# Kernel tuning notes

Hardware: AMD Instinct MI355X
Metric: run time of the kernel (lower is better)

## Reference

```python
import jax, jax.numpy as jnp
import numpy as np

P = 128; D = 128; A = 128
NS = D * A            # sinogram nodes
NP = P * P            # pixel nodes
N = NS + NP           # total graph nodes
EPS = 1e-5
_PNAMES = ["af_w1","af_b1","af_p1","af_bn_g","af_bn_b","af_w2","af_b2","af_p2","af_w3","af_b3","af_p3","af_w4","af_b4","af_p4","af_w5","af_b5","af_p5","gcn_w","gcn_b","sr_w1","sr_b1","sr_p1","sr_w2","sr_b2","sr_p2","sr_w3","sr_b3","sr_p3"]


def _conv(x, w, b, pad):
    y = jax.lax.conv_general_dilated(x, w, (1, 1), [(pad, pad), (pad, pad)],
                                     dimension_numbers=("NCHW", "OIHW", "NCHW"))
    return y + b[None, :, None, None]


def _prelu(x, a):
    return jnp.where(x >= 0, x, a * x)


def _bn(x, g, b):
    # BatchNorm2d in training mode: biased batch stats over (N,H,W)
    m = x.mean(axis=(0, 2, 3), keepdims=True)
    v = x.var(axis=(0, 2, 3), keepdims=True)
    return (x - m) * jax.lax.rsqrt(v + EPS) * g[None, :, None, None] + b[None, :, None, None]


def _forward(sino, edge_index, edge_weight, p):
    # AndrewCNN sinogram filter: 1 -> 64 -> 64 -> 64 -> 64 -> 8, 7x7 convs
    h = _prelu(_conv(sino, p["af_w1"], p["af_b1"], 3), p["af_p1"])
    h = _bn(h, p["af_bn_g"], p["af_bn_b"])
    h = _prelu(_conv(h, p["af_w2"], p["af_b2"], 3), p["af_p2"])
    h = _prelu(_conv(h, p["af_w3"], p["af_b3"], 3), p["af_p3"])
    h = _prelu(_conv(h, p["af_w4"], p["af_b4"], 3), p["af_p4"])
    h = _prelu(_conv(h, p["af_w5"], p["af_b5"], 3), p["af_p5"])   # [B,8,D,A]
    B, F = h.shape[0], h.shape[1]
    # build_nodes_features (source_to_target): sino nodes first, zero pixel nodes
    flat_sino = h.transpose(0, 2, 3, 1).reshape(B, NS, F)
    x = jnp.concatenate([flat_sino, jnp.zeros((B, NP, F), h.dtype)], axis=1)  # [B,N,8]
    # GCNConv(8,10): lin -> gcn_norm with self loops -> scatter-add at targets -> +bias
    xl = x @ p["gcn_w"]                                            # [B,N,10]
    row, col = edge_index[0], edge_index[1]
    loop = jnp.arange(N)
    row2 = jnp.concatenate([row, loop])
    col2 = jnp.concatenate([col, loop])
    w2 = jnp.concatenate([edge_weight, jnp.ones((N,), edge_weight.dtype)])
    deg = jnp.zeros((N,), xl.dtype).at[col2].add(w2)
    dis = jnp.where(deg > 0, jax.lax.rsqrt(jnp.maximum(deg, EPS * 0 + 1e-30)), 0.0)
    norm = dis[row2] * w2 * dis[col2]                              # [E+N]
    msgs = xl[:, row2, :] * norm[None, :, None]                    # [B,E+N,10]
    agg = jnp.zeros_like(xl).at[:, col2, :].add(msgs) + p["gcn_b"]
    # keep pixel nodes, reshape to image grid
    img = agg[:, NS:, :].transpose(0, 2, 1).reshape(B, -1, P, P)   # [B,10,P,P]
    # SRNET: 10 -> 64 (9x9) -> 32 (1x1) -> 1 (5x5)
    o = _prelu(_conv(img, p["sr_w1"], p["sr_b1"], 4), p["sr_p1"])
    o = _prelu(_conv(o,   p["sr_w2"], p["sr_b2"], 0), p["sr_p2"])
    o = _prelu(_conv(o,   p["sr_w3"], p["sr_b3"], 2), p["sr_p3"])
    return o


def setup_inputs() -> dict:
    f = jnp.float32
    ks = jax.random.split(jax.random.key(0), 16)
    B, E = 4, 2097152
    def rn(k, shape, s):
        return jax.random.normal(k, shape, f) * s
    inp = {
        "sino": jax.random.normal(ks[0], (B, 1, D, A), f),
        "edge_index": jax.random.randint(ks[1], (2, E), 0, N),
        "edge_weight": jax.random.uniform(ks[2], (E,), f),
    }
    kw = jax.random.split(ks[3], 9)
    inp["af_w1"] = rn(kw[0], (64, 1, 7, 7), 0.2)
    inp["af_w2"] = rn(kw[1], (64, 64, 7, 7), 0.03)
    inp["af_w3"] = rn(kw[2], (64, 64, 7, 7), 0.03)
    inp["af_w4"] = rn(kw[3], (64, 64, 7, 7), 0.03)
    inp["af_w5"] = rn(kw[4], (8, 64, 7, 7), 0.03)
    inp["gcn_w"] = rn(kw[5], (8, 10), 0.3)
    inp["sr_w1"] = rn(kw[6], (64, 10, 9, 9), 0.05)
    inp["sr_w2"] = rn(kw[7], (32, 64, 1, 1), 0.18)
    inp["sr_w3"] = rn(kw[8], (1, 32, 5, 5), 0.05)
    for nm, c in [("af_b1", 64), ("af_b2", 64), ("af_b3", 64), ("af_b4", 64), ("af_b5", 8), ("sr_b1", 64), ("sr_b2", 32), ("sr_b3", 1)]:
        inp[nm] = jnp.zeros((c,), f)
    inp["gcn_b"] = jnp.zeros((10,), f)
    inp["af_bn_g"] = jnp.ones((64,), f)
    inp["af_bn_b"] = jnp.zeros((64,), f)
    for nm in ["af_p1", "af_p2", "af_p3", "af_p4", "af_p5", "sr_p1", "sr_p2", "sr_p3"]:
        inp[nm] = jnp.array(0.25, f)
    return inp


def reference(sino, edge_index, edge_weight, af_w1, af_b1, af_p1, af_bn_g, af_bn_b, af_w2, af_b2, af_p2, af_w3, af_b3, af_p3, af_w4, af_b4, af_p4, af_w5, af_b5, af_p5, gcn_w, gcn_b, sr_w1, sr_b1, sr_p1, sr_w2, sr_b2, sr_p2, sr_w3, sr_b3, sr_p3):
    p = dict(zip(_PNAMES, (af_w1, af_b1, af_p1, af_bn_g, af_bn_b, af_w2, af_b2, af_p2, af_w3, af_b3, af_p3, af_w4, af_b4, af_p4, af_w5, af_b5, af_p5, gcn_w, gcn_b, sr_w1, sr_b1, sr_p1, sr_w2, sr_b2, sr_p2, sr_w3, sr_b3, sr_p3)))
    return _forward(sino, edge_index, edge_weight, p)
```

## Files before the change

kernel.cpp:

```cpp
#include <hip/hip_runtime.h>

static constexpr int NS = 16384;

typedef __attribute__((ext_vector_type(8))) short bf16x8;
typedef __attribute__((ext_vector_type(4))) float f32x4;

__device__ inline unsigned short bf16_rne(float x) {
  unsigned u = __float_as_uint(x);
  unsigned r = u + 0x7FFF + ((u >> 16) & 1);
  return (unsigned short)(r >> 16);
}

__global__ void k_wtrans(const float* __restrict__ w, float* __restrict__ wT,
                         int CO, int CI_IN, int CI_OUT, int KS) {
  int i = blockIdx.x * 256 + threadIdx.x;
  int tot = KS * KS * CI_OUT * CO;
  if (i >= tot) return;
  int co = i % CO;
  int r = i / CO;
  int ci = r % CI_OUT;
  int t = r / CI_OUT;
  int ky = t / KS, kx = t % KS;
  float v = 0.f;
  if (ci < CI_IN) v = w[((co * CI_IN + ci) * KS + ky) * KS + kx];
  wT[i] = v;
}

__global__ void k_wpack(const float* __restrict__ w, unsigned short* __restrict__ wpk) {
  int i = blockIdx.x * 256 + threadIdx.x;
  if (i >= 49 * 64 * 64) return;
  int co = i & 63, r = i >> 6;
  int ci = r & 63, tap = r >> 6;
  float v = w[(co * 64 + ci) * 49 + tap];
  unsigned short hi = bf16_rne(v);
  float hif = __uint_as_float((unsigned)hi << 16);
  unsigned short lo = bf16_rne(v - hif);
  int ks = ci >> 5, k32 = ci & 31;
  int lane = ((k32 >> 3) << 4) | (co & 15);
  int j = ci & 7, nt = co >> 4;
  size_t base = ((size_t)(((tap * 2 + ks) * 4 + nt) * 2) * 64 + lane) * 8 + j;
  wpk[base] = hi;
  wpk[base + 512] = lo;
}

__global__ void k_wpacks(const float* __restrict__ sw1,
                         unsigned short* __restrict__ wpk) {
  int i = blockIdx.x * 256 + threadIdx.x;
  if (i >= 360 * 512) return;
  int j = i & 7, l = (i >> 3) & 63, f = i >> 9;
  int sp = f & 1, nt = (f >> 1) & 3;
  int r3 = f >> 3, p = r3 % 5, ky = r3 / 5;
  int co = nt * 16 + (l & 15);
  int k = ((l >> 4) << 3) + j;
  int kx = 2 * p + (k >> 4);
  int ci = k & 15;
  float v = (ci < 10 && kx < 9) ? sw1[((co * 10 + ci) * 9 + ky) * 9 + kx] : 0.f;
  unsigned short hi = bf16_rne(v);
  unsigned short outv;
  if (sp == 0) {
    outv = hi;
  } else {
    float hif = __uint_as_float((unsigned)hi << 16);
    outv = bf16_rne(v - hif);
  }
  wpk[i] = outv;
}

__global__ __launch_bounds__(128) void k_conv1(
    const float* __restrict__ sino, const float* __restrict__ wT1,
    const float* __restrict__ b1, const float* __restrict__ p1,
    float* __restrict__ out) {
  int b = blockIdx.x >> 7, y = blockIdx.x & 127, x = threadIdx.x;
  float acc[64];
#pragma unroll
  for (int i = 0; i < 64; ++i) acc[i] = 0.f;
#pragma unroll
  for (int ky = 0; ky < 7; ++ky) {
    int yy = y + ky - 3;
#pragma unroll
    for (int kx = 0; kx < 7; ++kx) {
      int xx = x + kx - 3;
      float v = (yy >= 0 && yy < 128 && xx >= 0 && xx < 128)
                    ? sino[(b * 128 + yy) * 128 + xx]
                    : 0.f;
      const float* wr = wT1 + (ky * 7 + kx) * 64;
#pragma unroll
      for (int co = 0; co < 64; ++co) acc[co] += v * wr[co];
    }
  }
  float a = p1[0];
  float* op = out + ((size_t)(b * 134 + y + 3) * 134 + x + 3) * 64;
#pragma unroll
  for (int co = 0; co < 64; ++co) {
    float v = acc[co] + b1[co];
    op[co] = v >= 0.f ? v : a * v;
  }
}

__global__ __launch_bounds__(256) void k_bnstats(const float* __restrict__ x1p,
                                                 double* __restrict__ bnsum) {
  int c = threadIdx.x & 63, sl = threadIdx.x >> 6;
  double s = 0.0, q = 0.0;
  int base = blockIdx.x * 512 + sl * 128;
  for (int i = 0; i < 128; ++i) {
    int p = base + i;
    int b = p >> 14, y = (p >> 7) & 127, x = p & 127;
    double v = (double)x1p[((size_t)(b * 134 + y + 3) * 134 + x + 3) * 64 + c];
    s += v;
    q += v * v;
  }
  __shared__ double red[2][4][64];
  red[0][sl][c] = s;
  red[1][sl][c] = q;
  __syncthreads();
  if (sl == 0) {
    s = red[0][0][c] + red[0][1][c] + red[0][2][c] + red[0][3][c];
    q = red[1][0][c] + red[1][1][c] + red[1][2][c] + red[1][3][c];
    atomicAdd(&bnsum[c], s);
    atomicAdd(&bnsum[64 + c], q);
  }
}

__global__ void k_bnfinal(const double* __restrict__ bnsum, float* __restrict__ bnsc,
                          const float* __restrict__ g, const float* __restrict__ bb) {
  int c = threadIdx.x;
  if (c >= 64) return;
  double m = bnsum[c] * (1.0 / 65536.0);
  double v = bnsum[64 + c] * (1.0 / 65536.0) - m * m;
  double sc = (double)g[c] * rsqrt(v + 1e-5);
  bnsc[c] = (float)sc;
  bnsc[64 + c] = (float)((double)bb[c] - m * sc);
}

__global__ __launch_bounds__(256) void k_bnapply(float* __restrict__ x1p,
                                                 const float* __restrict__ bnsc) {
  int i = blockIdx.x * 256 + threadIdx.x;
  if (i >= 4 * 128 * 128 * 16) return;
  int g = i & 15, p = i >> 4;
  int b = p >> 14, y = (p >> 7) & 127, x = p & 127;
  float* ptr = x1p + ((size_t)(b * 134 + y + 3) * 134 + x + 3) * 64 + g * 4;
  float4 v = *(float4*)ptr;
  int c = g * 4;
  v.x = v.x * bnsc[c + 0] + bnsc[64 + c + 0];
  v.y = v.y * bnsc[c + 1] + bnsc[64 + c + 1];
  v.z = v.z * bnsc[c + 2] + bnsc[64 + c + 2];
  v.w = v.w * bnsc[c + 3] + bnsc[64 + c + 3];
  *(float4*)ptr = v;
}

__global__ __launch_bounds__(256) void k_convm(
    const float* __restrict__ in, const unsigned short* __restrict__ wpk,
    const float* __restrict__ bias, const float* __restrict__ alpha,
    float* __restrict__ out) {
  int b = blockIdx.x >> 7, y = blockIdx.x & 127;
  int tid = threadIdx.x, l = tid & 63;
  int wv = tid >> 6;
  int wbase = wv * 32;
  int lg = l >> 4, lm = l & 15;

  __shared__ unsigned short hbuf[2][134 * 40];
  __shared__ unsigned short lbuf[2][134 * 40];

  f32x4 acc[2][4];
#pragma unroll
  for (int mt = 0; mt < 2; ++mt)
#pragma unroll
    for (int nt = 0; nt < 4; ++nt) acc[mt][nt] = (f32x4){0.f, 0.f, 0.f, 0.f};

  for (int ch = 0; ch < 64; ch += 32) {
    auto stage = [&](int ky, int s) {
      const float* gin = in + ((size_t)(b * 134 + y + ky) * 134) * 64 + ch;
      for (int i = tid; i < 134 * 8; i += 256) {
        int px = i >> 3, q = i & 7;
        float4 v = *(const float4*)(gin + px * 64 + q * 4);
        unsigned short h0 = bf16_rne(v.x), h1 = bf16_rne(v.y);
        unsigned short h2 = bf16_rne(v.z), h3 = bf16_rne(v.w);
        unsigned short l0 = bf16_rne(v.x - __uint_as_float((unsigned)h0 << 16));
        unsigned short l1 = bf16_rne(v.y - __uint_as_float((unsigned)h1 << 16));
        unsigned short l2 = bf16_rne(v.z - __uint_as_float((unsigned)h2 << 16));
        unsigned short l3 = bf16_rne(v.w - __uint_as_float((unsigned)h3 << 16));
        *(ushort4*)&hbuf[s][px * 40 + q * 4] = make_ushort4(h0, h1, h2, h3);
        *(ushort4*)&lbuf[s][px * 40 + q * 4] = make_ushort4(l0, l1, l2, l3);
      }
    };
    stage(0, 0);
    __syncthreads();
    for (int ky = 0; ky < 7; ++ky) {
      if (ky < 6) stage(ky + 1, (ky + 1) & 1);
      int s = ky & 1;
#pragma unroll
      for (int kx = 0; kx < 7; ++kx) {
        int tap = ky * 7 + kx;
        const unsigned short* wt =
            wpk + (size_t)(tap * 2 + (ch >> 5)) * 8 * 512 + (size_t)l * 8;
        bf16x8 Bh[4], Bl[4];
#pragma unroll
        for (int nt = 0; nt < 4; ++nt) {
          Bh[nt] = *(const bf16x8*)(wt + (nt * 2 + 0) * 512);
          Bl[nt] = *(const bf16x8*)(wt + (nt * 2 + 1) * 512);
        }
#pragma unroll
        for (int mt = 0; mt < 2; ++mt) {
          int px = wbase + mt * 16 + lm + kx;
          bf16x8 Ah = *(const bf16x8*)&hbuf[s][px * 40 + lg * 8];
          bf16x8 Al = *(const bf16x8*)&lbuf[s][px * 40 + lg * 8];
#pragma unroll
          for (int nt = 0; nt < 4; ++nt) {
            acc[mt][nt] =
                __builtin_amdgcn_mfma_f32_16x16x32_bf16(Ah, Bh[nt], acc[mt][nt], 0, 0, 0);
            acc[mt][nt] =
                __builtin_amdgcn_mfma_f32_16x16x32_bf16(Ah, Bl[nt], acc[mt][nt], 0, 0, 0);
            acc[mt][nt] =
                __builtin_amdgcn_mfma_f32_16x16x32_bf16(Al, Bh[nt], acc[mt][nt], 0, 0, 0);
          }
        }
      }
      __syncthreads();
    }
  }
  float a = alpha[0];
#pragma unroll
  for (int mt = 0; mt < 2; ++mt)
#pragma unroll
    for (int nt = 0; nt < 4; ++nt)
#pragma unroll
      for (int r = 0; r < 4; ++r) {
        int px = wbase + mt * 16 + lg * 4 + r;
        int co = nt * 16 + lm;
        float v = acc[mt][nt][r] + bias[co];
        out[((size_t)(b * 134 + y + 3) * 134 + px + 3) * 64 + co] =
            v >= 0.f ? v : a * v;
      }
}

__global__ __launch_bounds__(256) void k_convs(
    const float* __restrict__ imgp, const unsigned short* __restrict__ wpk,
    const float* __restrict__ bias, const float* __restrict__ alpha,
    float* __restrict__ out) {
  int b = blockIdx.x >> 7, y = blockIdx.x & 127;
  int tid = threadIdx.x, l = tid & 63;
  int wv = tid >> 6, wbase = wv * 32;
  int lg = l >> 4, lm = l & 15;

  __shared__ unsigned short hbuf[2][137 * 20];
  __shared__ unsigned short lbuf[2][137 * 20];

  f32x4 acc[2][4];
#pragma unroll
  for (int mt = 0; mt < 2; ++mt)
#pragma unroll
    for (int nt = 0; nt < 4; ++nt) acc[mt][nt] = (f32x4){0.f, 0.f, 0.f, 0.f};

  auto stage = [&](int ky, int s) {
    const float* gin = imgp + ((size_t)(b * 136 + y + ky) * 136) * 16;
    for (int i = tid; i < 137 * 4; i += 256) {
      int px = i >> 2, q = i & 3;
      float4 v = (px < 136) ? *(const float4*)(gin + px * 16 + q * 4)
                            : make_float4(0.f, 0.f, 0.f, 0.f);
      unsigned short h0 = bf16_rne(v.x), h1 = bf16_rne(v.y);
      unsigned short h2 = bf16_rne(v.z), h3 = bf16_rne(v.w);
      unsigned short l0 = bf16_rne(v.x - __uint_as_float((unsigned)h0 << 16));
      unsigned short l1 = bf16_rne(v.y - __uint_as_float((unsigned)h1 << 16));
      unsigned short l2 = bf16_rne(v.z - __uint_as_float((unsigned)h2 << 16));
      unsigned short l3 = bf16_rne(v.w - __uint_as_float((unsigned)h3 << 16));
      *(ushort4*)&hbuf[s][px * 20 + q * 4] = make_ushort4(h0, h1, h2, h3);
      *(ushort4*)&lbuf[s][px * 20 + q * 4] = make_ushort4(l0, l1, l2, l3);
    }
  };
  stage(0, 0);
  __syncthreads();
  for (int ky = 0; ky < 9; ++ky) {
    if (ky < 8) stage(ky + 1, (ky + 1) & 1);
    int s = ky & 1;
#pragma unroll
    for (int p = 0; p < 5; ++p) {
      const unsigned short* wt =
          wpk + ((size_t)(ky * 5 + p) * 8) * 512 + (size_t)l * 8;
      bf16x8 Bh[4], Bl[4];
#pragma unroll
      for (int nt = 0; nt < 4; ++nt) {
        Bh[nt] = *(const bf16x8*)(wt + (nt * 2 + 0) * 512);
        Bl[nt] = *(const bf16x8*)(wt + (nt * 2 + 1) * 512);
      }
#pragma unroll
      for (int mt = 0; mt < 2; ++mt) {
        int px = wbase + mt * 16 + lm + 2 * p + (lg >> 1);
        bf16x8 Ah = *(const bf16x8*)&hbuf[s][px * 20 + (lg & 1) * 8];
        bf16x8 Al = *(const bf16x8*)&lbuf[s][px * 20 + (lg & 1) * 8];
#pragma unroll
        for (int nt = 0; nt < 4; ++nt) {
          acc[mt][nt] =
              __builtin_amdgcn_mfma_f32_16x16x32_bf16(Ah, Bh[nt], acc[mt][nt], 0, 0, 0);
          acc[mt][nt] =
              __builtin_amdgcn_mfma_f32_16x16x32_bf16(Ah, Bl[nt], acc[mt][nt], 0, 0, 0);
          acc[mt][nt] =
              __builtin_amdgcn_mfma_f32_16x16x32_bf16(Al, Bh[nt], acc[mt][nt], 0, 0, 0);
        }
      }
    }
    __syncthreads();
  }
  float a = alpha[0];
#pragma unroll
  for (int mt = 0; mt < 2; ++mt)
#pragma unroll
    for (int nt = 0; nt < 4; ++nt)
#pragma unroll
      for (int r = 0; r < 4; ++r) {
        int px = wbase + mt * 16 + lg * 4 + r;
        int co = nt * 16 + lm;
        float v = acc[mt][nt][r] + bias[co];
        out[((size_t)(b * 128 + y) * 128 + px) * 64 + co] = v >= 0.f ? v : a * v;
      }
}

template <int CIN, int COUT, int KS, int IN_H, int IN_W, int OUT_H, int OUT_W,
          int OUT_OFF, int STR, int CH, int NSPLIT>
__global__ __launch_bounds__(64 * NSPLIT) void k_conv3(
    const float* __restrict__ in, const float* __restrict__ wT,
    const float* __restrict__ bias, const float* __restrict__ alpha,
    float* __restrict__ out) {
  constexpr int C = COUT / NSPLIT;
  int b = blockIdx.x >> 6, y0 = (blockIdx.x & 63) * 2;
  int l = threadIdx.x & 63;
  int cob = __builtin_amdgcn_readfirstlane((int)(threadIdx.x >> 6) * C);
  __shared__ float sbuf[2][IN_W * STR];
  float acc[4][C];
#pragma unroll
  for (int r = 0; r < 4; ++r)
#pragma unroll
    for (int i = 0; i < C; ++i) acc[r][i] = 0.f;

  for (int ch = 0; ch < CIN; ch += CH) {
    auto stage = [&](int k) {
      const float* gin = in + ((size_t)(b * IN_H + y0 + k) * IN_W) * CIN + ch;
      float* dst = sbuf[k & 1];
      constexpr int N4 = IN_W * CH / 4;
      for (int i = threadIdx.x; i < N4; i += 64 * NSPLIT) {
        int xx = i / (CH / 4), c4 = (i - xx * (CH / 4)) * 4;
        float4 v = *(const float4*)(gin + (size_t)xx * CIN + c4);
        *(float4*)(dst + xx * STR + c4) = v;
      }
    };
    stage(0);
    stage(1);
    __syncthreads();
    for (int ky = 0; ky < KS; ++ky) {
      const float* sA = sbuf[ky & 1];
      const float* sB = sbuf[(ky + 1) & 1];
      for (int kx = 0; kx < KS; ++kx) {
        const float* wt = wT + ((size_t)(ky * KS + kx) * CIN + ch) * COUT + cob;
        const float* a0p = sA + (l + kx) * STR;
        const float* a1p = sA + (l + 64 + kx) * STR;
        const float* b0p = sB + (l + kx) * STR;
        const float* b1p = sB + (l + 64 + kx) * STR;
#pragma unroll
        for (int ci = 0; ci < CH; ci += 4) {
          float4 a0 = *(const float4*)(a0p + ci);
          float4 a1 = *(const float4*)(a1p + ci);
          float4 b0 = *(const float4*)(b0p + ci);
          float4 b1 = *(const float4*)(b1p + ci);
#pragma unroll
          for (int c = 0; c < 4; ++c) {
            const float* wr = wt + (size_t)(ci + c) * COUT;
            float va0 = ((const float*)&a0)[c], va1 = ((const float*)&a1)[c];
            float vb0 = ((const float*)&b0)[c], vb1 = ((const float*)&b1)[c];
#pragma unroll
            for (int co = 0; co < C; ++co) {
              float w = wr[co];
              acc[0][co] += va0 * w;
              acc[1][co] += va1 * w;
              acc[2][co] += vb0 * w;
              acc[3][co] += vb1 * w;
            }
          }
        }
      }
      __syncthreads();
      if (ky < KS - 1) {
        stage(ky + 2);
        __syncthreads();
      }
    }
  }
  float a = alpha[0];
#pragma unroll
  for (int r = 0; r < 2; ++r) {
    float* rowp =
        out + (((size_t)(b * OUT_H + y0 + r + OUT_OFF)) * OUT_W + OUT_OFF) * COUT + cob;
#pragma unroll
    for (int p = 0; p < 2; ++p) {
      float* op = rowp + (size_t)(l + p * 64) * COUT;
#pragma unroll
      for (int co = 0; co < C; ++co) {
        float v = acc[r * 2 + p][co] + bias[cob + co];
        op[co] = v >= 0.f ? v : a * v;
      }
    }
  }
}

template <int CIN, int COUT, int KS, int IN_H, int IN_W, int OUT_H, int OUT_W,
          int OUT_OFF, int STR, int NSPLIT>
__global__ __launch_bounds__(64 * NSPLIT) void k_conv2(
    const float* __restrict__ in, const float* __restrict__ wT,
    const float* __restrict__ bias, const float* __restrict__ alpha,
    float* __restrict__ out) {
  constexpr int C = COUT / NSPLIT;
  int b = blockIdx.x >> 7, y = blockIdx.x & 127;
  int l = threadIdx.x & 63;
  int cob = __builtin_amdgcn_readfirstlane((int)(threadIdx.x >> 6) * C);
  __shared__ float srow[IN_W * STR];
  float acc0[C], acc1[C];
#pragma unroll
  for (int i = 0; i < C; ++i) acc0[i] = acc1[i] = 0.f;

  for (int ky = 0; ky < KS; ++ky) {
    __syncthreads();
    const float* gin = in + (size_t)(b * IN_H + y + ky) * IN_W * CIN;
    constexpr int N4 = IN_W * CIN / 4;
    for (int i = threadIdx.x; i < N4; i += 64 * NSPLIT) {
      float4 v = *(const float4*)(gin + (size_t)i * 4);
      int xx = (i * 4) / CIN, cc = (i * 4) % CIN;
      *(float4*)(srow + xx * STR + cc) = v;
    }
    __syncthreads();
    for (int kx = 0; kx < KS; ++kx) {
      const float* wt = wT + ((size_t)(ky * KS + kx) * CIN) * COUT + cob;
      const float* s0 = srow + (l + kx) * STR;
      const float* s1 = srow + (l + 64 + kx) * STR;
      for (int ci = 0; ci < CIN; ci += 4) {
        float4 a0 = *(const float4*)(s0 + ci);
        float4 a1 = *(const float4*)(s1 + ci);
#pragma unroll
        for (int c = 0; c < 4; ++c) {
          float v0 = ((const float*)&a0)[c];
          float v1 = ((const float*)&a1)[c];
          const float* wr = wt + (size_t)(ci + c) * COUT;
#pragma unroll
          for (int co = 0; co < C; ++co) {
            float w = wr[co];
            acc0[co] += v0 * w;
            acc1[co] += v1 * w;
          }
        }
      }
    }
  }
  float a = alpha[0];
  float* rowp = out + ((size_t)(b * OUT_H + y + OUT_OFF) * OUT_W + OUT_OFF) * COUT + cob;
  float* op0 = rowp + (size_t)l * COUT;
  float* op1 = rowp + (size_t)(l + 64) * COUT;
#pragma unroll
  for (int co = 0; co < C; ++co) {
    float bi = bias[cob + co];
    float v0 = acc0[co] + bi;
    float v1 = acc1[co] + bi;
    op0[co] = v0 >= 0.f ? v0 : a * v0;
    op1[co] = v1 >= 0.f ? v1 : a * v1;
  }
}

__global__ __launch_bounds__(512, 4) void k_conv5gcn(
    const float* __restrict__ in, const float* __restrict__ wT5,
    const float* __restrict__ b5, const float* __restrict__ p5,
    const float* __restrict__ gw, float* __restrict__ xl) {
  int b = blockIdx.x >> 7, y = blockIdx.x & 127;
  int x = threadIdx.x & 127;
  int cig = __builtin_amdgcn_readfirstlane((int)(threadIdx.x >> 7));
  __shared__ float srow[134 * 68];
  __shared__ float red[4][128][8];
  float acc[8];
#pragma unroll
  for (int i = 0; i < 8; ++i) acc[i] = 0.f;

  for (int ky = 0; ky < 7; ++ky) {
    __syncthreads();
    const float* gin = in + (size_t)(b * 134 + y + ky) * 134 * 64;
    for (int i = threadIdx.x; i < 134 * 64; i += 512) {
      int xx = i >> 6, cc = i & 63;
      srow[xx * 68 + cc] = gin[i];
    }
    __syncthreads();
    for (int kx = 0; kx < 7; ++kx) {
      const float* wt = wT5 + (size_t)(ky * 7 + kx) * 64 * 8 + cig * 16 * 8;
      const float* sr = srow + (x + kx) * 68 + cig * 16;
#pragma unroll
      for (int ci = 0; ci < 16; ci += 4) {
        float4 iv = *(const float4*)(sr + ci);
#pragma unroll
        for (int c = 0; c < 4; ++c) {
          float vv = ((const float*)&iv)[c];
          const float* wr = wt + (ci + c) * 8;
#pragma unroll
          for (int co = 0; co < 8; ++co) acc[co] += vv * wr[co];
        }
      }
    }
  }
#pragma unroll
  for (int co = 0; co < 8; ++co) red[cig][x][co] = acc[co];
  __syncthreads();
  if (cig == 0) {
    float a = p5[0];
    float feat[8];
#pragma unroll
    for (int co = 0; co < 8; ++co) {
      float v = red[0][x][co] + red[1][x][co] + red[2][x][co] + red[3][x][co] + b5[co];
      feat[co] = v >= 0.f ? v : a * v;
    }
    float o[10];
#pragma unroll
    for (int f = 0; f < 10; ++f) o[f] = 0.f;
#pragma unroll
    for (int c = 0; c < 8; ++c) {
#pragma unroll
      for (int f = 0; f < 10; ++f) o[f] += feat[c] * gw[c * 10 + f];
    }
    float* op = xl + ((size_t)b * 16384 + y * 128 + x) * 10;
#pragma unroll
    for (int f = 0; f < 10; ++f) op[f] = o[f];
  }
}

template <int HALF>
__global__ __launch_bounds__(1024) void k_degp(
    const int* __restrict__ ei, const float* __restrict__ ew,
    float* __restrict__ pdeg, int* __restrict__ cnt, int* __restrict__ rank, int E) {
  __shared__ float degl[16384];
  for (int i = threadIdx.x; i < 16384; i += 1024) degl[i] = 0.f;
  __syncthreads();
  int chunk = (E + gridDim.x - 1) / gridDim.x;
  int base = blockIdx.x * chunk;
  int end = min(E, base + chunk);
  for (int e = base + (int)threadIdx.x; e < end; e += 1024) {
    int col = ei[E + e];
    float w = ew[e];
    if ((col >> 14) == HALF) atomicAdd(&degl[col & 16383], w);
    if (HALF == 1) {
      int row = ei[e];
      if (row < NS && col >= NS) rank[e] = atomicAdd(&cnt[col - NS], 1);
    }
  }
  __syncthreads();
  float* pd = pdeg + (size_t)blockIdx.x * 16384;
  for (int i = threadIdx.x; i < 16384; i += 1024) pd[i] = degl[i];
}

__global__ void k_dis2(const float* __restrict__ pdegA, const float* __restrict__ pdegB,
                       float* __restrict__ dis, int nb) {
  int n = blockIdx.x * 256 + threadIdx.x;
  if (n >= 2 * NS) return;
  const float* p = (n < NS ? pdegA : pdegB) + (n & 16383);
  float s = 1.0f;
  for (int b = 0; b < nb; ++b) s += p[(size_t)b * 16384];
  dis[n] = rsqrtf(s);
}

__global__ __launch_bounds__(1024) void k_scan(const int* __restrict__ cnt,
                                               int* __restrict__ ptr) {
  __shared__ int ps[1024];
  int tid = threadIdx.x;
  int base = tid * 16;
  int v[16];
  int s = 0;
#pragma unroll
  for (int k = 0; k < 16; ++k) {
    v[k] = s;
    s += cnt[base + k];
  }
  ps[tid] = s;
  __syncthreads();
  for (int off = 1; off < 1024; off <<= 1) {
    int t = (tid >= off) ? ps[tid - off] : 0;
    __syncthreads();
    ps[tid] += t;
    __syncthreads();
  }
  int chunkoff = (tid == 0) ? 0 : ps[tid - 1];
#pragma unroll
  for (int k = 0; k < 16; ++k) ptr[base + k] = chunkoff + v[k];
  if (tid == 1023) ptr[16384] = ps[1023];
}

__global__ void k_bucket2(const int* __restrict__ ei, const float* __restrict__ ew,
                          const float* __restrict__ dis, const int* __restrict__ ptr,
                          const int* __restrict__ rank, int* __restrict__ erow,
                          float* __restrict__ enrm, int E) {
  int e = blockIdx.x * 256 + threadIdx.x;
  if (e >= E) return;
  int row = ei[e], col = ei[E + e];
  if (row >= NS || col < NS) return;
  int cp = col - NS;
  int pos = ptr[cp] + rank[e];
  erow[pos] = row;
  enrm[pos] = dis[row] * ew[e] * dis[col];
}

__global__ __launch_bounds__(256) void k_gather(
    const int* __restrict__ ptr, const int* __restrict__ erow,
    const float* __restrict__ enrm, const float* __restrict__ xl,
    const float* __restrict__ gb, float* __restrict__ imgp) {
  int cp = blockIdx.x * 4 + (threadIdx.x >> 6);
  int l = threadIdx.x & 63;
  int b = l >> 4, f = l & 15;
  bool act = f < 10;
  float acc = 0.f;
  int s = ptr[cp], e1 = ptr[cp + 1];
  for (int e = s; e < e1; ++e) {
    int row = erow[e];
    float nrm = enrm[e];
    if (act) acc += xl[((size_t)b * 16384 + row) * 10 + f] * nrm;
  }
  if (act) {
    int y = cp >> 7, x = cp & 127;
    imgp[((size_t)(b * 136 + y + 4) * 136 + x + 4) * 16 + f] = acc + gb[f];
  }
}

extern "C" void kernel_launch(void* const* d_in, const int* in_sizes, int n_in,
                              void* d_out, int out_size, void* d_ws, size_t ws_size,
                              hipStream_t stream) {
  const float* sino = (const float*)d_in[0];
  const int* ei = (const int*)d_in[1];
  const float* ew = (const float*)d_in[2];
  const float* w1 = (const float*)d_in[3];
  const float* w2 = (const float*)d_in[4];
  const float* w3 = (const float*)d_in[5];
  const float* w4 = (const float*)d_in[6];
  const float* w5 = (const float*)d_in[7];
  const float* gw = (const float*)d_in[8];
  const float* sw1 = (const float*)d_in[9];
  const float* sw2 = (const float*)d_in[10];
  const float* sw3 = (const float*)d_in[11];
  const float* b1 = (const float*)d_in[12];
  const float* b2 = (const float*)d_in[13];
  const float* b3 = (const float*)d_in[14];
  const float* b4 = (const float*)d_in[15];
  const float* b5 = (const float*)d_in[16];
  const float* sb1 = (const float*)d_in[17];
  const float* sb2 = (const float*)d_in[18];
  const float* sb3 = (const float*)d_in[19];
  const float* gb = (const float*)d_in[20];
  const float* bng = (const float*)d_in[21];
  const float* bnb = (const float*)d_in[22];
  const float* p1 = (const float*)d_in[23];
  const float* p2 = (const float*)d_in[24];
  const float* p3 = (const float*)d_in[25];
  const float* p4 = (const float*)d_in[26];
  const float* p5 = (const float*)d_in[27];
  const float* sp1 = (const float*)d_in[28];
  const float* sp2 = (const float*)d_in[29];
  const float* sp3 = (const float*)d_in[30];
  const int E = in_sizes[2];

  char* ws = (char*)d_ws;
  size_t off = 0;
  auto alloc = [&](size_t bytes) {
    char* p = ws + off;
    off += (bytes + 255) & ~(size_t)255;
    return p;
  };
  float* x1p = (float*)alloc((size_t)4 * 134 * 134 * 64 * 4);
  float* x2p = (float*)alloc((size_t)4 * 134 * 134 * 64 * 4);
  unsigned short* wpk2 = (unsigned short*)alloc(401408 * 2);
  unsigned short* wpk3 = (unsigned short*)alloc(401408 * 2);
  unsigned short* wpk4 = (unsigned short*)alloc(401408 * 2);
  unsigned short* wpks1 = (unsigned short*)alloc(184320 * 2);
  float* wt1 = (float*)alloc(3136 * 4);
  float* wt5 = (float*)alloc(25088 * 4);
  float* wts2 = (float*)alloc(2048 * 4);
  float* wts3 = (float*)alloc(800 * 4);
  double* bnsum = (double*)alloc(128 * 8);
  float* bnsc = (float*)alloc(128 * 4);
  float* xl = (float*)alloc((size_t)4 * 16384 * 10 * 4);
  float* pdegA = (float*)alloc((size_t)128 * 16384 * 4);
  float* pdegB = (float*)alloc((size_t)128 * 16384 * 4);
  float* dis = (float*)alloc(32768 * 4);
  int* cnt = (int*)alloc(16384 * 4);
  int* ptr = (int*)alloc(16385 * 4);
  int* rank = (int*)alloc((size_t)E * 4);
  int* erow = (int*)alloc((size_t)E * 4);
  float* enrm = (float*)alloc((size_t)E * 4);
  float* imgp = (float*)alloc((size_t)4 * 136 * 136 * 16 * 4);
  float* s1 = (float*)alloc((size_t)4 * 128 * 128 * 64 * 4);
  float* s2p = (float*)alloc((size_t)4 * 132 * 132 * 32 * 4);

  hipMemsetAsync(x1p, 0, (size_t)4 * 134 * 134 * 64 * 4, stream);
  hipMemsetAsync(x2p, 0, (size_t)4 * 134 * 134 * 64 * 4, stream);
  hipMemsetAsync(bnsum, 0, 128 * 8, stream);
  hipMemsetAsync(cnt, 0, 16384 * 4, stream);
  hipMemsetAsync(imgp, 0, (size_t)4 * 136 * 136 * 16 * 4, stream);
  hipMemsetAsync(s2p, 0, (size_t)4 * 132 * 132 * 32 * 4, stream);

  k_wpack<<<784, 256, 0, stream>>>(w2, wpk2);
  k_wpack<<<784, 256, 0, stream>>>(w3, wpk3);
  k_wpack<<<784, 256, 0, stream>>>(w4, wpk4);
  k_wpacks<<<720, 256, 0, stream>>>(sw1, wpks1);
  k_wtrans<<<13, 256, 0, stream>>>(w1, wt1, 64, 1, 1, 7);
  k_wtrans<<<98, 256, 0, stream>>>(w5, wt5, 8, 64, 64, 7);
  k_wtrans<<<8, 256, 0, stream>>>(sw2, wts2, 32, 64, 64, 1);
  k_wtrans<<<4, 256, 0, stream>>>(sw3, wts3, 1, 32, 32, 5);

  k_conv1<<<512, 128, 0, stream>>>(sino, wt1, b1, p1, x1p);
  k_bnstats<<<128, 256, 0, stream>>>(x1p, bnsum);
  k_bnfinal<<<1, 64, 0, stream>>>(bnsum, bnsc, bng, bnb);
  k_bnapply<<<4096, 256, 0, stream>>>(x1p, bnsc);

  k_convm<<<512, 256, 0, stream>>>(x1p, wpk2, b2, p2, x2p);
  k_convm<<<512, 256, 0, stream>>>(x2p, wpk3, b3, p3, x1p);
  k_convm<<<512, 256, 0, stream>>>(x1p, wpk4, b4, p4, x2p);
  k_conv5gcn<<<512, 512, 0, stream>>>(x2p, wt5, b5, p5, gw, xl);

  k_degp<0><<<128, 1024, 0, stream>>>(ei, ew, pdegA, cnt, rank, E);
  k_degp<1><<<128, 1024, 0, stream>>>(ei, ew, pdegB, cnt, rank, E);
  k_dis2<<<128, 256, 0, stream>>>(pdegA, pdegB, dis, 128);
  k_scan<<<1, 1024, 0, stream>>>(cnt, ptr);
  k_bucket2<<<(E + 255) / 256, 256, 0, stream>>>(ei, ew, dis, ptr, rank, erow, enrm, E);
  k_gather<<<4096, 256, 0, stream>>>(ptr, erow, enrm, xl, gb, imgp);

  k_convs<<<512, 256, 0, stream>>>(imgp, wpks1, sb1, sp1, s1);
  k_conv3<64, 32, 1, 128, 128, 132, 132, 2, 36, 32, 8>
      <<<256, 512, 0, stream>>>(s1, wts2, sb2, sp2, s2p);
  k_conv2<32, 1, 5, 132, 132, 128, 128, 0, 36, 1>
      <<<512, 64, 0, stream>>>(s2p, wts3, sb3, sp3, (float*)d_out);
}
```

Measured before the change: 675.1 us.

## Compute two output rows per block in middle convs sharing staged input rows

Each k_convm block now produces two adjacent output rows, with waves split across rows and 64-pixel halves, so staged input rows and loaded weight fragments are reused across twice as many MFMAs. Staging moves to a ring of two rows loaded between synchronized compute phases, and the grid is halved. This cuts redundant global loads and bf16 splitting but removes the stage/compute overlap, doubles accumulator registers, and halves the number of blocks, which may underfill the GPU.

Result: slower. 721.8 us (+6.9%).

```diff
diff --git a/kernel.cpp b/kernel.cpp
--- a/kernel.cpp
+++ b/kernel.cpp
@@ -152,24 +152,26 @@
     const float* __restrict__ in, const unsigned short* __restrict__ wpk,
     const float* __restrict__ bias, const float* __restrict__ alpha,
     float* __restrict__ out) {
-  int b = blockIdx.x >> 7, y = blockIdx.x & 127;
+  int b = blockIdx.x >> 6, y0 = (blockIdx.x & 63) * 2;
   int tid = threadIdx.x, l = tid & 63;
   int wv = tid >> 6;
-  int wbase = wv * 32;
+  int row = wv >> 1, pxb = (wv & 1) * 64;
   int lg = l >> 4, lm = l & 15;
 
   __shared__ unsigned short hbuf[2][134 * 40];
   __shared__ unsigned short lbuf[2][134 * 40];
 
-  f32x4 acc[2][4];
-#pragma unroll
-  for (int mt = 0; mt < 2; ++mt)
+  f32x4 acc[4][4];
+#pragma unroll
+  for (int mt = 0; mt < 4; ++mt)
 #pragma unroll
     for (int nt = 0; nt < 4; ++nt) acc[mt][nt] = (f32x4){0.f, 0.f, 0.f, 0.f};
 
   for (int ch = 0; ch < 64; ch += 32) {
-    auto stage = [&](int ky, int s) {
-      const float* gin = in + ((size_t)(b * 134 + y + ky) * 134) * 64 + ch;
+    auto stage = [&](int k) {
+      const float* gin = in + ((size_t)(b * 134 + y0 + k) * 134) * 64 + ch;
+      unsigned short* hd = hbuf[k & 1];
+      unsigned short* ld = lbuf[k & 1];
       for (int i = tid; i < 134 * 8; i += 256) {
         int px = i >> 3, q = i & 7;
         float4 v = *(const float4*)(gin + px * 64 + q * 4);
@@ -179,15 +181,17 @@
         unsigned short l1 = bf16_rne(v.y - __uint_as_float((unsigned)h1 << 16));
         unsigned short l2 = bf16_rne(v.z - __uint_as_float((unsigned)h2 << 16));
         unsigned short l3 = bf16_rne(v.w - __uint_as_float((unsigned)h3 << 16));
-        *(ushort4*)&hbuf[s][px * 40 + q * 4] = make_ushort4(h0, h1, h2, h3);
-        *(ushort4*)&lbuf[s][px * 40 + q * 4] = make_ushort4(l0, l1, l2, l3);
+        *(ushort4*)&hd[px * 40 + q * 4] = make_ushort4(h0, h1, h2, h3);
+        *(ushort4*)&ld[px * 40 + q * 4] = make_ushort4(l0, l1, l2, l3);
       }
     };
-    stage(0, 0);
+    stage(0);
+    stage(1);
     __syncthreads();
     for (int ky = 0; ky < 7; ++ky) {
-      if (ky < 6) stage(ky + 1, (ky + 1) & 1);
-      int s = ky & 1;
+      int s = (ky + row) & 1;
+      const unsigned short* hb = hbuf[s];
+      const unsigned short* lb = lbuf[s];
 #pragma unroll
       for (int kx = 0; kx < 7; ++kx) {
         int tap = ky * 7 + kx;
@@ -200,10 +204,10 @@
           Bl[nt] = *(const bf16x8*)(wt + (nt * 2 + 1) * 512);
         }
 #pragma unroll
-        for (int mt = 0; mt < 2; ++mt) {
-          int px = wbase + mt * 16 + lm + kx;
-          bf16x8 Ah = *(const bf16x8*)&hbuf[s][px * 40 + lg * 8];
-          bf16x8 Al = *(const bf16x8*)&lbuf[s][px * 40 + lg * 8];
+        for (int mt = 0; mt < 4; ++mt) {
+          int px = pxb + mt * 16 + lm + kx;
+          bf16x8 Ah = *(const bf16x8*)&hb[px * 40 + lg * 8];
+          bf16x8 Al = *(const bf16x8*)&lb[px * 40 + lg * 8];
 #pragma unroll
           for (int nt = 0; nt < 4; ++nt) {
             acc[mt][nt] =
@@ -216,19 +220,23 @@
         }
       }
       __syncthreads();
+      if (ky < 6) {
+        stage(ky + 2);
+        __syncthreads();
+      }
     }
   }
   float a = alpha[0];
 #pragma unroll
-  for (int mt = 0; mt < 2; ++mt)
+  for (int mt = 0; mt < 4; ++mt)
 #pragma unroll
     for (int nt = 0; nt < 4; ++nt)
 #pragma unroll
       for (int r = 0; r < 4; ++r) {
-        int px = wbase + mt * 16 + lg * 4 + r;
+        int px = pxb + mt * 16 + lg * 4 + r;
         int co = nt * 16 + lm;
         float v = acc[mt][nt][r] + bias[co];
-        out[((size_t)(b * 134 + y + 3) * 134 + px + 3) * 64 + co] =
+        out[((size_t)(b * 134 + y0 + row + 3) * 134 + px + 3) * 64 + co] =
             v >= 0.f ? v : a * v;
       }
 }
@@ -707,9 +715,9 @@
   k_bnfinal<<<1, 64, 0, stream>>>(bnsum, bnsc, bng, bnb);
   k_bnapply<<<4096, 256, 0, stream>>>(x1p, bnsc);
 
-  k_convm<<<512, 256, 0, stream>>>(x1p, wpk2, b2, p2, x2p);
-  k_convm<<<512, 256, 0, stream>>>(x2p, wpk3, b3, p3, x1p);
-  k_convm<<<512, 256, 0, stream>>>(x1p, wpk4, b4, p4, x2p);
+  k_convm<<<256, 256, 0, stream>>>(x1p, wpk2, b2, p2, x2p);
+  k_convm<<<256, 256, 0, stream>>>(x2p, wpk3, b3, p3, x1p);
+  k_convm<<<256, 256, 0, stream>>>(x1p, wpk4, b4, p4, x2p);
   k_conv5gcn<<<512, 512, 0, stream>>>(x2p, wt5, b5, p5, gw, xl);
 
   k_degp<0><<<128, 1024, 0, stream>>>(ei, ew, pdegA, cnt, rank, E);
```

## Split conv taps across waves with full-row tiles and LDS reduction

Applied to the files above, without the earlier changes.

The 64-channel 7x7 conv kernel now gives each wave a subset of the filter taps covering the whole 128-pixel output row, instead of one 32-pixel slice across all taps. Input rows are staged two at a time into a tighter LDS layout with a 36-element stride, replacing the per-row double buffer. Partial sums from the four waves are then combined through LDS before bias and PReLU are applied. The aim is to cut redundant weight loads per wave and change LDS bank behaviour, at the cost of 128 accumulator registers per thread, extra barriers, a reduction pass, and uneven tap counts across waves (14 or 7 taps per stage).

New measurement: 795.4 us. +17.8%, slower.

```diff
diff --git a/kernel.cpp b/kernel.cpp
--- a/kernel.cpp
+++ b/kernel.cpp
@@ -154,43 +154,47 @@
     float* __restrict__ out) {
   int b = blockIdx.x >> 7, y = blockIdx.x & 127;
   int tid = threadIdx.x, l = tid & 63;
-  int wv = tid >> 6;
-  int wbase = wv * 32;
+  int wv = __builtin_amdgcn_readfirstlane(tid >> 6);
   int lg = l >> 4, lm = l & 15;
 
-  __shared__ unsigned short hbuf[2][134 * 40];
-  __shared__ unsigned short lbuf[2][134 * 40];
-
-  f32x4 acc[2][4];
-#pragma unroll
-  for (int mt = 0; mt < 2; ++mt)
+  __shared__ unsigned short sm[2][2][4824];
+
+  f32x4 acc[8][4];
+#pragma unroll
+  for (int mt = 0; mt < 8; ++mt)
 #pragma unroll
     for (int nt = 0; nt < 4; ++nt) acc[mt][nt] = (f32x4){0.f, 0.f, 0.f, 0.f};
 
+#pragma unroll 1
   for (int ch = 0; ch < 64; ch += 32) {
-    auto stage = [&](int ky, int s) {
-      const float* gin = in + ((size_t)(b * 134 + y + ky) * 134) * 64 + ch;
-      for (int i = tid; i < 134 * 8; i += 256) {
-        int px = i >> 3, q = i & 7;
-        float4 v = *(const float4*)(gin + px * 64 + q * 4);
+#pragma unroll 1
+    for (int p = 0; p < 4; ++p) {
+      int r0 = 2 * p;
+      int nky = (p < 3) ? 2 : 1;
+      int tot = nky * 134 * 8;
+      for (int i = tid; i < tot; i += 256) {
+        int row = (i >= 134 * 8) ? 1 : 0;
+        int rem = i - row * 134 * 8;
+        int px = rem >> 3, q = rem & 7;
+        const float* gp =
+            in + ((size_t)(b * 134 + y + r0 + row) * 134 + px) * 64 + ch + q * 4;
+        float4 v = *(const float4*)gp;
         unsigned short h0 = bf16_rne(v.x), h1 = bf16_rne(v.y);
         unsigned short h2 = bf16_rne(v.z), h3 = bf16_rne(v.w);
         unsigned short l0 = bf16_rne(v.x - __uint_as_float((unsigned)h0 << 16));
         unsigned short l1 = bf16_rne(v.y - __uint_as_float((unsigned)h1 << 16));
         unsigned short l2 = bf16_rne(v.z - __uint_as_float((unsigned)h2 << 16));
         unsigned short l3 = bf16_rne(v.w - __uint_as_float((unsigned)h3 << 16));
-        *(ushort4*)&hbuf[s][px * 40 + q * 4] = make_ushort4(h0, h1, h2, h3);
-        *(ushort4*)&lbuf[s][px * 40 + q * 4] = make_ushort4(l0, l1, l2, l3);
-      }
-    };
-    stage(0, 0);
-    __syncthreads();
-    for (int ky = 0; ky < 7; ++ky) {
-      if (ky < 6) stage(ky + 1, (ky + 1) & 1);
-      int s = ky & 1;
-#pragma unroll
-      for (int kx = 0; kx < 7; ++kx) {
-        int tap = ky * 7 + kx;
+        int off = px * 36 + q * 4;
+        *(ushort4*)&sm[0][row][off] = make_ushort4(h0, h1, h2, h3);
+        *(ushort4*)&sm[1][row][off] = make_ushort4(l0, l1, l2, l3);
+      }
+      __syncthreads();
+      int ntaps = nky * 7;
+      for (int t = wv; t < ntaps; t += 4) {
+        int kys = (t >= 7) ? 1 : 0;
+        int kx = t - kys * 7;
+        int tap = (r0 + kys) * 7 + kx;
         const unsigned short* wt =
             wpk + (size_t)(tap * 2 + (ch >> 5)) * 8 * 512 + (size_t)l * 8;
         bf16x8 Bh[4], Bl[4];
@@ -199,11 +203,13 @@
           Bh[nt] = *(const bf16x8*)(wt + (nt * 2 + 0) * 512);
           Bl[nt] = *(const bf16x8*)(wt + (nt * 2 + 1) * 512);
         }
-#pragma unroll
-        for (int mt = 0; mt < 2; ++mt) {
-          int px = wbase + mt * 16 + lm + kx;
-          bf16x8 Ah = *(const bf16x8*)&hbuf[s][px * 40 + lg * 8];
-          bf16x8 Al = *(const bf16x8*)&lbuf[s][px * 40 + lg * 8];
+        const unsigned short* hb = sm[0][kys];
+        const unsigned short* lb = sm[1][kys];
+#pragma unroll
+        for (int mt = 0; mt < 8; ++mt) {
+          int px = mt * 16 + lm + kx;
+          bf16x8 Ah = *(const bf16x8*)&hb[px * 36 + lg * 8];
+          bf16x8 Al = *(const bf16x8*)&lb[px * 36 + lg * 8];
 #pragma unroll
           for (int nt = 0; nt < 4; ++nt) {
             acc[mt][nt] =
@@ -218,19 +224,42 @@
       __syncthreads();
     }
   }
+
+  float* redf = (float*)&sm[0][0][0];
   float a = alpha[0];
 #pragma unroll
-  for (int mt = 0; mt < 2; ++mt)
-#pragma unroll
-    for (int nt = 0; nt < 4; ++nt)
-#pragma unroll
-      for (int r = 0; r < 4; ++r) {
-        int px = wbase + mt * 16 + lg * 4 + r;
-        int co = nt * 16 + lm;
-        float v = acc[mt][nt][r] + bias[co];
-        out[((size_t)(b * 134 + y + 3) * 134 + px + 3) * 64 + co] =
-            v >= 0.f ? v : a * v;
-      }
+  for (int c = 0; c < 4; ++c) {
+#pragma unroll
+    for (int mloc = 0; mloc < 2; ++mloc) {
+#pragma unroll
+      for (int nt = 0; nt < 4; ++nt)
+        *(f32x4*)&redf[((wv * 64 + l) * 2 + mloc) * 16 + nt * 4] = acc[2 * c + mloc][nt];
+    }
+    __syncthreads();
+#pragma unroll
+    for (int mloc = 0; mloc < 2; ++mloc) {
+      int m = 2 * c + mloc;
+      if (wv == (m & 3)) {
+#pragma unroll
+        for (int nt = 0; nt < 4; ++nt) {
+          f32x4 s = *(f32x4*)&redf[((0 * 64 + l) * 2 + mloc) * 16 + nt * 4];
+#pragma unroll
+          for (int w2 = 1; w2 < 4; ++w2)
+            s += *(f32x4*)&redf[((w2 * 64 + l) * 2 + mloc) * 16 + nt * 4];
+          int co = nt * 16 + lm;
+          float bi = bias[co];
+#pragma unroll
+          for (int r = 0; r < 4; ++r) {
+            int px = m * 16 + lg * 4 + r;
+            float v = s[r] + bi;
+            out[((size_t)(b * 134 + y + 3) * 134 + px + 3) * 64 + co] =
+                v >= 0.f ? v : a * v;
+          }
+        }
+      }
+    }
+    __syncthreads();
+  }
 }
 
 __global__ __launch_bounds__(256) void k_convs(
```
